# Optimization experiments

Hardware: AMD Instinct MI355X
Metric: run time of the kernel (lower is better)

The kernel has to match this reference:

```python
import jax, jax.numpy as jnp
import numpy as np

DIM = 3072
H = 24
HD = DIM // H  # 128
B = 1
IMG = 2048
TXT = 256


def _apply_rope(x, cos, sin):
    # x: [B, H, S, D]; cos/sin: [S, D]. Diffusers-style interleaved rotate-half:
    # pairs (x0, x1) -> (x0*c - x1*s, x1*c + x0*s)
    x1 = x[..., 0::2]
    x2 = x[..., 1::2]
    x_rot = jnp.stack([-x2, x1], axis=-1).reshape(x.shape)
    return x * cos + x_rot * sin


def setup_inputs() -> dict:
    key = jax.random.key(0)
    ks = jax.random.split(key, 26)

    def w(k):
        return jax.random.normal(k, (DIM, DIM), jnp.float32) * 0.02

    def b(k):
        return jax.random.normal(k, (DIM,), jnp.float32) * 0.02

    return {
        "image_hidden_states": jax.random.normal(ks[0], (B, IMG, DIM), jnp.float32),
        "text_hidden_states": jax.random.normal(ks[1], (B, TXT, DIM), jnp.float32),
        "img_cos": jax.random.uniform(ks[2], (IMG, HD), jnp.float32),
        "img_sin": jax.random.uniform(ks[3], (IMG, HD), jnp.float32),
        "txt_cos": jax.random.uniform(ks[4], (TXT, HD), jnp.float32),
        "txt_sin": jax.random.uniform(ks[5], (TXT, HD), jnp.float32),
        "Wq": w(ks[6]), "bq": b(ks[7]),
        "Wk": w(ks[8]), "bk": b(ks[9]),
        "Wv": w(ks[10]), "bv": b(ks[11]),
        "Waq": w(ks[12]), "baq": b(ks[13]),
        "Wak": w(ks[14]), "bak": b(ks[15]),
        "Wav": w(ks[16]), "bav": b(ks[17]),
        "Wo": w(ks[18]), "bo": b(ks[19]),
        "Wao": w(ks[20]), "bao": b(ks[21]),
    }


def reference(image_hidden_states, text_hidden_states, img_cos, img_sin,
              txt_cos, txt_sin, Wq, bq, Wk, bk, Wv, bv, Waq, baq, Wak, bak,
              Wav, bav, Wo, bo, Wao, bao):
    Bz, Si, D = image_hidden_states.shape
    St = text_hidden_states.shape[1]

    def proj(x, W, b):  # torch nn.Linear: x @ W.T + b
        return x @ W.T + b

    def heads(x, S):  # [B,S,D] -> [B,H,S,HD]
        return x.reshape(Bz, S, H, HD).transpose(0, 2, 1, 3)

    q_img = heads(proj(image_hidden_states, Wq, bq), Si)
    k_img = heads(proj(image_hidden_states, Wk, bk), Si)
    v_img = heads(proj(image_hidden_states, Wv, bv), Si)
    q_txt = heads(proj(text_hidden_states, Waq, baq), St)
    k_txt = heads(proj(text_hidden_states, Wak, bak), St)
    v_txt = heads(proj(text_hidden_states, Wav, bav), St)

    q_img = _apply_rope(q_img, img_cos, img_sin)
    k_img = _apply_rope(k_img, img_cos, img_sin)
    q_txt = _apply_rope(q_txt, txt_cos, txt_sin)
    k_txt = _apply_rope(k_txt, txt_cos, txt_sin)

    # joint sequence: text first, then image
    q = jnp.concatenate([q_txt, q_img], axis=2)
    k = jnp.concatenate([k_txt, k_img], axis=2)
    v = jnp.concatenate([v_txt, v_img], axis=2)

    scale = HD ** -0.5
    scores = jnp.einsum('bhqd,bhkd->bhqk', q, k) * scale  # [B,H,S,S]
    attn = jax.nn.softmax(scores, axis=-1)
    out = jnp.einsum('bhqk,bhkd->bhqd', attn, v)
    out = out.transpose(0, 2, 1, 3).reshape(Bz, St + Si, D)

    txt_out = out[:, :St] @ Wao.T + bao
    img_out = out[:, St:] @ Wo.T + bo
    return (img_out, txt_out)
```

## Files before the change

kernel.cpp:

```cpp
#include <hip/hip_runtime.h>
#include <cstdint>
#include <cstddef>

typedef __bf16 bf16x8 __attribute__((ext_vector_type(8)));
typedef float  f32x4  __attribute__((ext_vector_type(4)));

#define S_TXT 256
#define S_IMG 2048
#define S_TOT 2304
#define NHEAD 24
#define HDIM  128
#define DMODEL 3072

static constexpr size_t SZ_QKV  = (size_t)NHEAD * S_TOT * HDIM;
static constexpr size_t SZ_AO   = (size_t)S_TOT * DMODEL;
static constexpr size_t SZ_XIMG = (size_t)S_IMG * DMODEL;
static constexpr size_t SZ_XTXT = (size_t)S_TXT * DMODEL;
static constexpr size_t SZ_W    = (size_t)DMODEL * DMODEL;

__device__ __forceinline__ f32x4 mfma16(bf16x8 a, bf16x8 b, f32x4 c) {
  return __builtin_amdgcn_mfma_f32_16x16x32_bf16(a, b, c, 0, 0, 0);
}

__global__ __launch_bounds__(256) void cvt_f32_bf16(const float* __restrict__ in,
                                                    __bf16* __restrict__ out, int n) {
  int i = (blockIdx.x * 256 + threadIdx.x) * 8;
  if (i + 8 > n) return;
  f32x4 a = *(const f32x4*)(in + i);
  f32x4 b = *(const f32x4*)(in + i + 4);
  bf16x8 r;
  r[0]=(__bf16)a[0]; r[1]=(__bf16)a[1]; r[2]=(__bf16)a[2]; r[3]=(__bf16)a[3];
  r[4]=(__bf16)b[0]; r[5]=(__bf16)b[1]; r[6]=(__bf16)b[2]; r[7]=(__bf16)b[3];
  *(bf16x8*)(out + i) = r;
}

struct CWArgs { const float* s[6]; __bf16* d[6]; };
__global__ __launch_bounds__(256) void cvt_w(CWArgs a) {
  const float* in = a.s[blockIdx.y];
  __bf16* out = a.d[blockIdx.y];
  size_t i = ((size_t)blockIdx.x * 256 + threadIdx.x) * 8;
  f32x4 x = *(const f32x4*)(in + i);
  f32x4 y = *(const f32x4*)(in + i + 4);
  bf16x8 r;
  r[0]=(__bf16)x[0]; r[1]=(__bf16)x[1]; r[2]=(__bf16)x[2]; r[3]=(__bf16)x[3];
  r[4]=(__bf16)y[0]; r[5]=(__bf16)y[1]; r[6]=(__bf16)y[2]; r[7]=(__bf16)y[3];
  *(bf16x8*)(out + i) = r;
}

__global__ __launch_bounds__(256) void rope_kernel(__bf16* __restrict__ Qb, __bf16* __restrict__ Kb,
    const float* __restrict__ icos, const float* __restrict__ isin,
    const float* __restrict__ tcos, const float* __restrict__ tsin) {
  size_t idx = ((size_t)blockIdx.x * 256 + threadIdx.x) * 8;
  __bf16* X; float mult;
  if (blockIdx.y) { X = Kb; mult = 1.0f; }
  else            { X = Qb; mult = 0.08838834764831845f; }
  int d = (int)(idx & 127);
  int s = (int)((idx >> 7) % S_TOT);
  const float *cp, *sp; int ss;
  if (s < S_TXT) { cp = tcos; sp = tsin; ss = s; }
  else           { cp = icos; sp = isin; ss = s - S_TXT; }
  const float* cb = cp + (size_t)ss * HDIM + d;
  const float* sb = sp + (size_t)ss * HDIM + d;
  f32x4 c0 = *(const f32x4*)(cb);
  f32x4 c1 = *(const f32x4*)(cb + 4);
  f32x4 s0 = *(const f32x4*)(sb);
  f32x4 s1 = *(const f32x4*)(sb + 4);
  bf16x8 x = *(const bf16x8*)(X + idx);
  float xf[8];
  #pragma unroll
  for (int j = 0; j < 8; ++j) xf[j] = (float)x[j];
  bf16x8 o;
  o[0] = (__bf16)((xf[0]*c0[0] - xf[1]*s0[0]) * mult);
  o[1] = (__bf16)((xf[1]*c0[1] + xf[0]*s0[1]) * mult);
  o[2] = (__bf16)((xf[2]*c0[2] - xf[3]*s0[2]) * mult);
  o[3] = (__bf16)((xf[3]*c0[3] + xf[2]*s0[3]) * mult);
  o[4] = (__bf16)((xf[4]*c1[0] - xf[5]*s1[0]) * mult);
  o[5] = (__bf16)((xf[5]*c1[1] + xf[4]*s1[1]) * mult);
  o[6] = (__bf16)((xf[6]*c1[2] - xf[7]*s1[2]) * mult);
  o[7] = (__bf16)((xf[7]*c1[3] + xf[6]*s1[3]) * mult);
  *(bf16x8*)(X + idx) = o;
}

__global__ __launch_bounds__(128) void transpose_v(const __bf16* __restrict__ V,
                                                   __bf16* __restrict__ Vt) {
  int h = blockIdx.y, s0 = blockIdx.x * 64, d = threadIdx.x;
  const __bf16* src = V + ((size_t)h * S_TOT + s0) * HDIM + d;
  __bf16 tmp[64];
  #pragma unroll
  for (int k = 0; k < 64; ++k) tmp[k] = src[(size_t)k * HDIM];
  __bf16* dst = Vt + ((size_t)h * HDIM + d) * S_TOT + s0;
  #pragma unroll
  for (int k = 0; k < 8; ++k) {
    bf16x8 v;
    #pragma unroll
    for (int j = 0; j < 8; ++j) v[j] = tmp[k*8 + j];
    *(bf16x8*)(dst + k*8) = v;
  }
}

struct GBArgs {
  const __bf16* A;
  const __bf16* W0[3];
  const __bf16* W1[3];
  const float* b0[3]; const float* b1[3];
  void* O0[3]; void* O1[3];
};

template<int MODE>
__global__ __launch_bounds__(256) void gemm_bf(GBArgs ga) {
  const int tid = threadIdx.x;
  const int lane = tid & 63, wave = tid >> 6;
  const int wr = wave >> 1, wc = wave & 1;
  const int g = lane >> 4, lr = lane & 15;
  const int x7 = lr & 7;

  const int hw = (int)blockIdx.x;
  const int xcd = hw & 7, idx = hw >> 3;
  const int bx = idx % 18;
  const int nglob = (MODE == 0) ? (xcd * 9 + idx / 18) : (xcd * 3 + idx / 18);
  const int wsel = (MODE == 0) ? nglob / 24 : 0;
  const int ny   = (MODE == 0) ? nglob % 24 : nglob;
  const int m0 = bx * 128;
  const int n0 = ny * 128;
  const bool txt = (MODE == 0) ? (m0 >= S_IMG) : (m0 < S_TXT);
  const __bf16* Wf  = txt ? ga.W1[wsel] : ga.W0[wsel];
  const float* bias = txt ? ga.b1[wsel] : ga.b0[wsel];

  __shared__ __align__(16) __bf16 As[128 * 64];
  __shared__ __align__(16) __bf16 Bs[128 * 64];

  const int sr8 = lane >> 3;
  const int sch = (lane & 7) ^ sr8;
  const __bf16* Ap = ga.A + (size_t)(m0 + wave * 8 + sr8) * DMODEL + sch * 8;
  const __bf16* Bp = Wf   + (size_t)(n0 + wave * 8 + sr8) * DMODEL + sch * 8;

  f32x4 acc[4][4];
  #pragma unroll
  for (int i = 0; i < 4; ++i)
    #pragma unroll
    for (int j = 0; j < 4; ++j) acc[i][j] = (f32x4){0.f,0.f,0.f,0.f};

#define GLD(dst, srcp) { \
    _Pragma("unroll") \
    for (int i_ = 0; i_ < 4; ++i_) \
      __builtin_amdgcn_global_load_lds( \
          (const __attribute__((address_space(1))) void*)((srcp) + (size_t)i_ * 32 * DMODEL), \
          (__attribute__((address_space(3))) void*)((char*)(dst) + i_ * 4096 + wave * 1024), \
          16, 0, 0); }

  for (int kt = 0; kt < DMODEL / 64; ++kt) {
    GLD(As, Ap + kt * 64);
    GLD(Bs, Bp + kt * 64);
    __syncthreads();
    #pragma unroll
    for (int ks = 0; ks < 2; ++ks) {
      bf16x8 af[4], bf[4];
      #pragma unroll
      for (int i = 0; i < 4; ++i)
        af[i] = *(const bf16x8*)((char*)As + (wr*64 + i*16 + lr) * 128 + (((ks*4 + g) ^ x7) << 4));
      #pragma unroll
      for (int j = 0; j < 4; ++j)
        bf[j] = *(const bf16x8*)((char*)Bs + (wc*64 + j*16 + lr) * 128 + (((ks*4 + g) ^ x7) << 4));
      __builtin_amdgcn_s_setprio(1);
      #pragma unroll
      for (int i = 0; i < 4; ++i)
        #pragma unroll
        for (int j = 0; j < 4; ++j)
          acc[i][j] = mfma16(af[i], bf[j], acc[i][j]);
      __builtin_amdgcn_s_setprio(0);
    }
    __syncthreads();
  }
#undef GLD

  float bv[4];
  #pragma unroll
  for (int j = 0; j < 4; ++j) bv[j] = bias[n0 + wc*64 + j*16 + lr];

  if (MODE == 0) {
    __bf16* Qp = (__bf16*)(txt ? ga.O1[wsel] : ga.O0[wsel]);
    const int sbase = txt ? (m0 - S_IMG) : (m0 + S_TXT);
    #pragma unroll
    for (int i = 0; i < 4; ++i)
      #pragma unroll
      for (int j = 0; j < 4; ++j)
        #pragma unroll
        for (int r = 0; r < 4; ++r) {
          int s  = sbase + wr*64 + i*16 + g*4 + r;
          int hd = wc*64 + j*16 + lr;
          Qp[((size_t)ny * S_TOT + s) * HDIM + hd] = (__bf16)(acc[i][j][r] + bv[j]);
        }
  } else {
    float* Cf = (float*)(txt ? ga.O1[0] : ga.O0[0]);
    const int rbase = txt ? m0 : (m0 - S_TXT);
    #pragma unroll
    for (int i = 0; i < 4; ++i)
      #pragma unroll
      for (int j = 0; j < 4; ++j)
        #pragma unroll
        for (int r = 0; r < 4; ++r) {
          int m = rbase + wr*64 + i*16 + g*4 + r;
          int n = n0 + wc*64 + j*16 + lr;
          Cf[(size_t)m * DMODEL + n] = acc[i][j][r] + bv[j];
        }
  }
}

struct GArgs {
  const __bf16* A;
  const float* W0[3]; const float* W1[3];
  const float* b0[3]; const float* b1[3];
  void* O0[3]; void* O1[3];
};

#define NT 48

template<int MODE>
__global__ __launch_bounds__(256, 1) void gemm_all(GArgs ga) {
  const int tid = threadIdx.x;
  const int lane = tid & 63, wave = tid >> 6;
  const int wr = wave >> 1, wc = wave & 1;
  const int g = lane >> 4, lr = lane & 15;
  const int x7 = lr & 7;

  const int hw = (int)blockIdx.x;
  const int xcd = hw & 7, idx = hw >> 3;
  const int bx = idx % 18;
  const int nglob = (MODE == 0) ? (xcd * 9 + idx / 18) : (xcd * 3 + idx / 18);
  const int wsel = (MODE == 0) ? nglob / 24 : 0;
  const int ny   = (MODE == 0) ? nglob % 24 : nglob;
  const int m0 = bx * 128;
  const int n0 = ny * 128;
  const bool txt = (MODE == 0) ? (m0 >= S_IMG) : (m0 < S_TXT);
  const float* Wf   = txt ? ga.W1[wsel] : ga.W0[wsel];
  const float* bias = txt ? ga.b1[wsel] : ga.b0[wsel];

  __shared__ __align__(16) __bf16 As[2][128 * 64];
  __shared__ __align__(16) __bf16 Bs[128 * 64];

  const int sr8 = lane >> 3;
  const int sch = (lane & 7) ^ sr8;
  const __bf16* Ap = ga.A + (size_t)(m0 + wave * 8 + sr8) * DMODEL + sch * 8;

  const int wrow = tid >> 3;
  const int wch  = tid & 7;
  const float* Bp = Wf + (size_t)(n0 + wrow) * DMODEL + wch * 8;
  const int bwoff = wrow * 128 + ((wch ^ (wrow & 7)) << 4);

  f32x4 acc[4][4];
  #pragma unroll
  for (int i = 0; i < 4; ++i)
    #pragma unroll
    for (int j = 0; j < 4; ++j) acc[i][j] = (f32x4){0.f,0.f,0.f,0.f};

  f32x4 pre[4][2];

#define VSEP asm volatile("" ::: "memory")
#define ISSUE_A(kt, buf) { \
    const __bf16* Apk = Ap + (kt) * 64; \
    char* dst = (char*)(&As[(buf)][0]) + wave * 1024; \
    _Pragma("unroll") \
    for (int i_ = 0; i_ < 4; ++i_) \
      __builtin_amdgcn_global_load_lds( \
          (const __attribute__((address_space(1))) void*)(Apk + (size_t)i_ * 32 * DMODEL), \
          (__attribute__((address_space(3))) void*)(dst + i_ * 4096), 16, 0, 0); }
#define ISSUE_B(kt) { \
    const float* Bpk = Bp + (kt) * 64; \
    _Pragma("unroll") \
    for (int p_ = 0; p_ < 4; ++p_) { \
      pre[p_][0] = *(const f32x4*)(Bpk + (size_t)p_ * 32 * DMODEL); \
      pre[p_][1] = *(const f32x4*)(Bpk + (size_t)p_ * 32 * DMODEL + 4); } }
#define WRITE_B() { \
    _Pragma("unroll") \
    for (int p_ = 0; p_ < 4; ++p_) { \
      bf16x8 bw_; \
      _Pragma("unroll") \
      for (int j_ = 0; j_ < 4; ++j_) { \
        bw_[j_]     = (__bf16)pre[p_][0][j_]; \
        bw_[4 + j_] = (__bf16)pre[p_][1][j_]; } \
      *(bf16x8*)((char*)Bs + p_ * 4096 + bwoff) = bw_; } }
#define COMPUTE(buf) { \
    _Pragma("unroll") \
    for (int ks_ = 0; ks_ < 2; ++ks_) { \
      bf16x8 af_[4], bf_[4]; \
      _Pragma("unroll") \
      for (int i_ = 0; i_ < 4; ++i_) \
        af_[i_] = *(const bf16x8*)((char*)(&As[(buf)][0]) + (wr*64 + i_*16 + lr) * 128 + (((ks_*4 + g) ^ x7) << 4)); \
      _Pragma("unroll") \
      for (int j_ = 0; j_ < 4; ++j_) \
        bf_[j_] = *(const bf16x8*)((char*)Bs + (wc*64 + j_*16 + lr) * 128 + (((ks_*4 + g) ^ x7) << 4)); \
      __builtin_amdgcn_s_setprio(1); \
      _Pragma("unroll") \
      for (int i_ = 0; i_ < 4; ++i_) \
        _Pragma("unroll") \
        for (int j_ = 0; j_ < 4; ++j_) \
          acc[i_][j_] = mfma16(af_[i_], bf_[j_], acc[i_][j_]); \
      __builtin_amdgcn_s_setprio(0); } }

  ISSUE_B(0);        VSEP;
  ISSUE_A(0, 0);     VSEP;
  asm volatile("s_waitcnt vmcnt(4)" ::: "memory");
  WRITE_B();
  asm volatile("s_waitcnt vmcnt(0) lgkmcnt(0)" ::: "memory");
  __builtin_amdgcn_s_barrier();
  VSEP;

  for (int t = 0; t < NT - 2; t += 2) {
    ISSUE_A(t + 1, 1);  VSEP;
    ISSUE_B(t + 1);     VSEP;
    COMPUTE(0);
    __builtin_amdgcn_s_barrier();
    asm volatile("s_waitcnt vmcnt(0)" ::: "memory");
    WRITE_B();
    asm volatile("s_waitcnt lgkmcnt(0)" ::: "memory");
    __builtin_amdgcn_s_barrier();
    VSEP;
    ISSUE_A(t + 2, 0);  VSEP;
    ISSUE_B(t + 2);     VSEP;
    COMPUTE(1);
    __builtin_amdgcn_s_barrier();
    asm volatile("s_waitcnt vmcnt(0)" ::: "memory");
    WRITE_B();
    asm volatile("s_waitcnt lgkmcnt(0)" ::: "memory");
    __builtin_amdgcn_s_barrier();
    VSEP;
  }

  ISSUE_A(NT - 1, 1);  VSEP;
  ISSUE_B(NT - 1);     VSEP;
  COMPUTE(0);
  __builtin_amdgcn_s_barrier();
  asm volatile("s_waitcnt vmcnt(0)" ::: "memory");
  WRITE_B();
  asm volatile("s_waitcnt lgkmcnt(0)" ::: "memory");
  __builtin_amdgcn_s_barrier();
  COMPUTE(1);

#undef VSEP
#undef ISSUE_A
#undef ISSUE_B
#undef WRITE_B
#undef COMPUTE

  float bv[4];
  #pragma unroll
  for (int j = 0; j < 4; ++j) bv[j] = bias[n0 + wc*64 + j*16 + lr];

  if (MODE == 0) {
    __bf16* Qp = (__bf16*)(txt ? ga.O1[wsel] : ga.O0[wsel]);
    const int sbase = txt ? (m0 - S_IMG) : (m0 + S_TXT);
    #pragma unroll
    for (int i = 0; i < 4; ++i)
      #pragma unroll
      for (int j = 0; j < 4; ++j)
        #pragma unroll
        for (int r = 0; r < 4; ++r) {
          int s  = sbase + wr*64 + i*16 + g*4 + r;
          int hd = wc*64 + j*16 + lr;
          Qp[((size_t)ny * S_TOT + s) * HDIM + hd] = (__bf16)(acc[i][j][r] + bv[j]);
        }
  } else {
    float* Cf = (float*)(txt ? ga.O1[0] : ga.O0[0]);
    const int rbase = txt ? m0 : (m0 - S_TXT);
    #pragma unroll
    for (int i = 0; i < 4; ++i)
      #pragma unroll
      for (int j = 0; j < 4; ++j)
        #pragma unroll
        for (int r = 0; r < 4; ++r) {
          int m = rbase + wr*64 + i*16 + g*4 + r;
          int n = n0 + wc*64 + j*16 + lr;
          Cf[(size_t)m * DMODEL + n] = acc[i][j][r] + bv[j];
        }
  }
}

__global__ __launch_bounds__(256, 2) void flash_attn(
    const __bf16* __restrict__ Qg, const __bf16* __restrict__ Kg,
    const __bf16* __restrict__ Vt, __bf16* __restrict__ Og)
{
  const int h = blockIdx.y;
  const int q0 = blockIdx.x * 64;
  const int tid = threadIdx.x;
  const int lane = tid & 63, wave = tid >> 6;
  const int g = lane >> 4, lr = lane & 15;
  const int x7 = lr & 7;

  __shared__ __align__(16) __bf16 Kl[64 * 128];
  __shared__ __align__(16) __bf16 Vl[128 * 64];
  __shared__ __align__(16) __bf16 Pl[4][16 * 64];
  char* Kc = (char*)Kl;
  char* Vc = (char*)Vl;
  char* Pc = (char*)&Pl[wave][0];

  bf16x8 qf[4];
  {
    const __bf16* qp = Qg + ((size_t)h * S_TOT + q0 + wave*16 + lr) * HDIM + g * 8;
    #pragma unroll
    for (int kb = 0; kb < 4; ++kb) qf[kb] = *(const bf16x8*)(qp + kb * 32);
  }

  f32x4 acc[8];
  #pragma unroll
  for (int i = 0; i < 8; ++i) acc[i] = (f32x4){0.f,0.f,0.f,0.f};
  float mrow[4] = {-__builtin_inff(), -__builtin_inff(), -__builtin_inff(), -__builtin_inff()};
  float lrow[4] = {0.f, 0.f, 0.f, 0.f};

  const int krow = tid >> 4, kc = tid & 15;
  const int vrow = tid >> 3, vc = tid & 7;
  const __bf16* Kbase = Kg + (size_t)h * S_TOT * HDIM;
  const __bf16* Vbase = Vt + (size_t)h * HDIM * S_TOT;

  const int kwoff = krow * 256 + ((kc ^ (krow & 7)) << 4);
  const int vwoff = vrow * 128 + ((vc ^ (vrow & 7)) << 4);

  bf16x8 kreg[4], vreg[4];
  #pragma unroll
  for (int i = 0; i < 4; ++i) {
    kreg[i] = *(const bf16x8*)(Kbase + (size_t)(i*16 + krow) * HDIM + kc * 8);
    vreg[i] = *(const bf16x8*)(Vbase + (size_t)(i*32 + vrow) * S_TOT + vc * 8);
  }

  for (int t = 0; t < S_TOT / 64; ++t) {
    asm volatile("" ::: "memory");
    __builtin_amdgcn_s_barrier();
    asm volatile("" ::: "memory");
    #pragma unroll
    for (int i = 0; i < 4; ++i) {
      *(bf16x8*)(Kc + kwoff + i * 4096) = kreg[i];
      *(bf16x8*)(Vc + vwoff + i * 4096) = vreg[i];
    }
    if (t + 1 < S_TOT / 64) {
      int kv1 = (t + 1) * 64;
      #pragma unroll
      for (int i = 0; i < 4; ++i) {
        kreg[i] = *(const bf16x8*)(Kbase + (size_t)(kv1 + i*16 + krow) * HDIM + kc * 8);
        vreg[i] = *(const bf16x8*)(Vbase + (size_t)(i*32 + vrow) * S_TOT + kv1 + vc * 8);
      }
    }
    asm volatile("s_waitcnt lgkmcnt(0)" ::: "memory");
    __builtin_amdgcn_s_barrier();
    asm volatile("" ::: "memory");

    f32x4 sc[4];
    __builtin_amdgcn_s_setprio(1);
    #pragma unroll
    for (int kb = 0; kb < 4; ++kb) {
      f32x4 s4 = (f32x4){0.f,0.f,0.f,0.f};
      #pragma unroll
      for (int dk = 0; dk < 4; ++dk) {
        bf16x8 kf = *(const bf16x8*)(Kc + (kb*16 + lr) * 256 + (((dk*4 + g) ^ x7) << 4));
        s4 = mfma16(qf[dk], kf, s4);
      }
      sc[kb] = s4;
    }
    __builtin_amdgcn_s_setprio(0);

    float alpha[4];
    #pragma unroll
    for (int r = 0; r < 4; ++r) {
      float mx = fmaxf(fmaxf(sc[0][r], sc[1][r]), fmaxf(sc[2][r], sc[3][r]));
      mx = fmaxf(mx, __shfl_xor(mx, 1));
      mx = fmaxf(mx, __shfl_xor(mx, 2));
      mx = fmaxf(mx, __shfl_xor(mx, 4));
      mx = fmaxf(mx, __shfl_xor(mx, 8));
      float mn = fmaxf(mrow[r], mx);
      float al = __expf(mrow[r] - mn);
      mrow[r] = mn;
      float ps = 0.f;
      #pragma unroll
      for (int kb = 0; kb < 4; ++kb) {
        float p = __expf(sc[kb][r] - mn);
        sc[kb][r] = p;
        ps += p;
      }
      ps += __shfl_xor(ps, 1); ps += __shfl_xor(ps, 2);
      ps += __shfl_xor(ps, 4); ps += __shfl_xor(ps, 8);
      lrow[r] = lrow[r] * al + ps;
      alpha[r] = al;
    }

    #pragma unroll
    for (int kb = 0; kb < 4; ++kb)
      #pragma unroll
      for (int r = 0; r < 4; ++r) {
        int row = g*4 + r;
        *(__bf16*)(Pc + (((row * 128) + (kb*16 + lr) * 2) ^ ((row & 7) << 4))) = (__bf16)sc[kb][r];
      }

    #pragma unroll
    for (int db = 0; db < 8; ++db)
      #pragma unroll
      for (int r = 0; r < 4; ++r) acc[db][r] *= alpha[r];

    bf16x8 ap0 = *(const bf16x8*)(Pc + ((lr * 128 + g * 16) ^ (x7 << 4)));
    bf16x8 ap1 = *(const bf16x8*)(Pc + ((lr * 128 + (4 + g) * 16) ^ (x7 << 4)));
    __builtin_amdgcn_s_setprio(1);
    #pragma unroll
    for (int db = 0; db < 8; ++db) {
      bf16x8 v0 = *(const bf16x8*)(Vc + (db*16 + lr) * 128 + ((g ^ x7) << 4));
      bf16x8 v1 = *(const bf16x8*)(Vc + (db*16 + lr) * 128 + (((4 + g) ^ x7) << 4));
      acc[db] = mfma16(ap0, v0, acc[db]);
      acc[db] = mfma16(ap1, v1, acc[db]);
    }
    __builtin_amdgcn_s_setprio(0);
  }

  float rinv[4];
  #pragma unroll
  for (int r = 0; r < 4; ++r) rinv[r] = 1.f / lrow[r];
  #pragma unroll
  for (int db = 0; db < 8; ++db)
    #pragma unroll
    for (int r = 0; r < 4; ++r) {
      int s = q0 + wave*16 + g*4 + r;
      Og[(size_t)s * DMODEL + h * HDIM + db*16 + lr] = (__bf16)(acc[db][r] * rinv[r]);
    }
}

extern "C" void kernel_launch(void* const* d_in, const int* in_sizes, int n_in,
                              void* d_out, int out_size, void* d_ws, size_t ws_size,
                              hipStream_t stream) {
  const float* x_img   = (const float*)d_in[0];
  const float* x_txt   = (const float*)d_in[1];
  const float* img_cos = (const float*)d_in[2];
  const float* img_sin = (const float*)d_in[3];
  const float* txt_cos = (const float*)d_in[4];
  const float* txt_sin = (const float*)d_in[5];
  const float* Wq  = (const float*)d_in[6];  const float* bq  = (const float*)d_in[7];
  const float* Wk  = (const float*)d_in[8];  const float* bk  = (const float*)d_in[9];
  const float* Wv  = (const float*)d_in[10]; const float* bv  = (const float*)d_in[11];
  const float* Waq = (const float*)d_in[12]; const float* baq = (const float*)d_in[13];
  const float* Wak = (const float*)d_in[14]; const float* bak = (const float*)d_in[15];
  const float* Wav = (const float*)d_in[16]; const float* bav = (const float*)d_in[17];
  const float* Wo  = (const float*)d_in[18]; const float* bo  = (const float*)d_in[19];
  const float* Wao = (const float*)d_in[20]; const float* bao = (const float*)d_in[21];

  __bf16* ws = (__bf16*)d_ws;
  __bf16* Qb  = ws;
  __bf16* Kb  = Qb + SZ_QKV;
  __bf16* Vb  = Kb + SZ_QKV;
  __bf16* Vtb = Vb + SZ_QKV;
  __bf16* AO  = Vtb + SZ_QKV;
  __bf16* XI  = AO + SZ_AO;
  __bf16* XT  = XI + SZ_XIMG;
  __bf16* Wbf = XI + SZ_AO;

  const size_t need_big = (5 * SZ_QKV + SZ_AO + 6 * SZ_W) * sizeof(__bf16);
  const bool big = ws_size >= need_big;

  float* out_img = (float*)d_out;
  float* out_txt = out_img + (size_t)S_IMG * DMODEL;

  cvt_f32_bf16<<<dim3((unsigned)(SZ_XIMG/2048)), 256, 0, stream>>>(x_img, XI, (int)SZ_XIMG);
  cvt_f32_bf16<<<dim3((unsigned)(SZ_XTXT/2048)), 256, 0, stream>>>(x_txt, XT, (int)SZ_XTXT);

  if (big) {
    CWArgs cw{};
    const float* wsrc[6] = {Wq, Wk, Wv, Waq, Wak, Wav};
    for (int i = 0; i < 6; ++i) { cw.s[i] = wsrc[i]; cw.d[i] = Wbf + (size_t)i * SZ_W; }
    cvt_w<<<dim3((unsigned)(SZ_W/2048), 6), 256, 0, stream>>>(cw);

    GBArgs gb{};
    gb.A = XI;
    gb.W0[0] = Wbf;            gb.W0[1] = Wbf + SZ_W;     gb.W0[2] = Wbf + 2*SZ_W;
    gb.W1[0] = Wbf + 3*SZ_W;   gb.W1[1] = Wbf + 4*SZ_W;   gb.W1[2] = Wbf + 5*SZ_W;
    gb.b0[0] = bq;  gb.b0[1] = bk;  gb.b0[2] = bv;
    gb.b1[0] = baq; gb.b1[1] = bak; gb.b1[2] = bav;
    gb.O0[0] = Qb;  gb.O0[1] = Kb;  gb.O0[2] = Vb;
    gb.O1[0] = Qb;  gb.O1[1] = Kb;  gb.O1[2] = Vb;
    gemm_bf<0><<<dim3(1296), 256, 0, stream>>>(gb);
  } else {
    GArgs gq{};
    gq.A = XI;
    gq.W0[0] = Wq;  gq.W0[1] = Wk;  gq.W0[2] = Wv;
    gq.W1[0] = Waq; gq.W1[1] = Wak; gq.W1[2] = Wav;
    gq.b0[0] = bq;  gq.b0[1] = bk;  gq.b0[2] = bv;
    gq.b1[0] = baq; gq.b1[1] = bak; gq.b1[2] = bav;
    gq.O0[0] = Qb;  gq.O0[1] = Kb;  gq.O0[2] = Vb;
    gq.O1[0] = Qb;  gq.O1[1] = Kb;  gq.O1[2] = Vb;
    gemm_all<0><<<dim3(1296), 256, 0, stream>>>(gq);
  }

  rope_kernel<<<dim3(3456, 2), 256, 0, stream>>>(Qb, Kb, img_cos, img_sin, txt_cos, txt_sin);
  transpose_v<<<dim3(36, 24), 128, 0, stream>>>(Vb, Vtb);
  flash_attn<<<dim3(36, 24), 256, 0, stream>>>(Qb, Kb, Vtb, AO);

  if (big) {
    CWArgs cw{};
    cw.s[0] = Wo;  cw.d[0] = Wbf;
    cw.s[1] = Wao; cw.d[1] = Wbf + SZ_W;
    cvt_w<<<dim3((unsigned)(SZ_W/2048), 2), 256, 0, stream>>>(cw);

    GBArgs go{};
    go.A = AO;
    go.W0[0] = Wbf;       go.W1[0] = Wbf + SZ_W;
    go.b0[0] = bo;  go.b1[0] = bao;
    go.O0[0] = out_img; go.O1[0] = out_txt;
    gemm_bf<1><<<dim3(432), 256, 0, stream>>>(go);
  } else {
    GArgs go{};
    go.A = AO;
    go.W0[0] = Wo;  go.W1[0] = Wao;
    go.b0[0] = bo;  go.b1[0] = bao;
    go.O0[0] = out_img; go.O1[0] = out_txt;
    gemm_all<1><<<dim3(432), 256, 0, stream>>>(go);
  }

  (void)in_sizes; (void)n_in; (void)out_size;
}
```

Before: 473.8 us.

## Fuse RoPE and V transpose into QKV GEMM epilogue, use exp2 softmax

The QKV projection epilogue now applies RoPE, with the Q scale folded in, to Q and K directly. It also writes V already transposed, so in the bf16 path the separate rope and transpose kernels and their extra global round trips go away. The log2(e) factor is folded into the Q scale so the attention softmax can use exp2f instead of __expf. The trade-off is an epilogue that does scattered fp32 cos/sin loads, shuffles and strided bf16x4 V stores, which may cost more than the launches saved.

```diff
diff --git a/kernel.cpp b/kernel.cpp
--- a/kernel.cpp
+++ b/kernel.cpp
@@ -3,6 +3,7 @@
 #include <cstddef>
 
 typedef __bf16 bf16x8 __attribute__((ext_vector_type(8)));
+typedef __bf16 bf16x4 __attribute__((ext_vector_type(4)));
 typedef float  f32x4  __attribute__((ext_vector_type(4)));
 
 #define S_TXT 256
@@ -17,6 +18,8 @@
 static constexpr size_t SZ_XIMG = (size_t)S_IMG * DMODEL;
 static constexpr size_t SZ_XTXT = (size_t)S_TXT * DMODEL;
 static constexpr size_t SZ_W    = (size_t)DMODEL * DMODEL;
+
+#define QSCALE (0.08838834764831845f * 1.4426950408889634f)
 
 __device__ __forceinline__ f32x4 mfma16(bf16x8 a, bf16x8 b, f32x4 c) {
   return __builtin_amdgcn_mfma_f32_16x16x32_bf16(a, b, c, 0, 0, 0);
@@ -53,7 +56,7 @@
   size_t idx = ((size_t)blockIdx.x * 256 + threadIdx.x) * 8;
   __bf16* X; float mult;
   if (blockIdx.y) { X = Kb; mult = 1.0f; }
-  else            { X = Qb; mult = 0.08838834764831845f; }
+  else            { X = Qb; mult = QSCALE; }
   int d = (int)(idx & 127);
   int s = (int)((idx >> 7) % S_TOT);
   const float *cp, *sp; int ss;
@@ -104,6 +107,8 @@
   const __bf16* W1[3];
   const float* b0[3]; const float* b1[3];
   void* O0[3]; void* O1[3];
+  const float* icos; const float* isin;
+  const float* tcos; const float* tsin;
 };
 
 template<int MODE>
@@ -178,18 +183,47 @@
   for (int j = 0; j < 4; ++j) bv[j] = bias[n0 + wc*64 + j*16 + lr];
 
   if (MODE == 0) {
-    __bf16* Qp = (__bf16*)(txt ? ga.O1[wsel] : ga.O0[wsel]);
-    const int sbase = txt ? (m0 - S_IMG) : (m0 + S_TXT);
-    #pragma unroll
-    for (int i = 0; i < 4; ++i)
-      #pragma unroll
-      for (int j = 0; j < 4; ++j)
+    const int head = ny;
+    if (wsel == 2) {
+      __bf16* Vt = (__bf16*)ga.O0[2];
+      const int sbase = txt ? (m0 - S_IMG) : (m0 + S_TXT);
+      #pragma unroll
+      for (int i = 0; i < 4; ++i) {
+        const int s0 = sbase + wr*64 + i*16 + g*4;
         #pragma unroll
-        for (int r = 0; r < 4; ++r) {
-          int s  = sbase + wr*64 + i*16 + g*4 + r;
-          int hd = wc*64 + j*16 + lr;
-          Qp[((size_t)ny * S_TOT + s) * HDIM + hd] = (__bf16)(acc[i][j][r] + bv[j]);
+        for (int j = 0; j < 4; ++j) {
+          const int hd = wc*64 + j*16 + lr;
+          bf16x4 pk;
+          #pragma unroll
+          for (int r = 0; r < 4; ++r) pk[r] = (__bf16)(acc[i][j][r] + bv[j]);
+          *(bf16x4*)(Vt + ((size_t)(head * HDIM + hd)) * S_TOT + s0) = pk;
         }
+      }
+    } else {
+      __bf16* Qp = (__bf16*)ga.O0[wsel];
+      const float* tc = txt ? ga.tcos : ga.icos;
+      const float* ts = txt ? ga.tsin : ga.isin;
+      const float mult = (wsel == 0) ? QSCALE : 1.0f;
+      const int sbase = txt ? (m0 - S_IMG) : (m0 + S_TXT);
+      const int tbase = txt ? (m0 - S_IMG) : m0;
+      #pragma unroll
+      for (int i = 0; i < 4; ++i)
+        #pragma unroll
+        for (int j = 0; j < 4; ++j) {
+          const int hd = wc*64 + j*16 + lr;
+          #pragma unroll
+          for (int r = 0; r < 4; ++r) {
+            const int soff = wr*64 + i*16 + g*4 + r;
+            float v = acc[i][j][r] + bv[j];
+            float p = __shfl_xor(v, 1);
+            const size_t trow = (size_t)(tbase + soff) * HDIM + hd;
+            float c  = tc[trow];
+            float sn = ts[trow];
+            float o = (lr & 1) ? (v * c + p * sn) : (v * c - p * sn);
+            Qp[((size_t)head * S_TOT + (sbase + soff)) * HDIM + hd] = (__bf16)(o * mult);
+          }
+        }
+    }
   } else {
     float* Cf = (float*)(txt ? ga.O1[0] : ga.O0[0]);
     const int rbase = txt ? m0 : (m0 - S_TXT);
@@ -465,12 +499,12 @@
       mx = fmaxf(mx, __shfl_xor(mx, 4));
       mx = fmaxf(mx, __shfl_xor(mx, 8));
       float mn = fmaxf(mrow[r], mx);
-      float al = __expf(mrow[r] - mn);
+      float al = exp2f(mrow[r] - mn);
       mrow[r] = mn;
       float ps = 0.f;
       #pragma unroll
       for (int kb = 0; kb < 4; ++kb) {
-        float p = __expf(sc[kb][r] - mn);
+        float p = exp2f(sc[kb][r] - mn);
         sc[kb][r] = p;
         ps += p;
       }
@@ -567,8 +601,9 @@
     gb.W1[0] = Wbf + 3*SZ_W;   gb.W1[1] = Wbf + 4*SZ_W;   gb.W1[2] = Wbf + 5*SZ_W;
     gb.b0[0] = bq;  gb.b0[1] = bk;  gb.b0[2] = bv;
     gb.b1[0] = baq; gb.b1[1] = bak; gb.b1[2] = bav;
-    gb.O0[0] = Qb;  gb.O0[1] = Kb;  gb.O0[2] = Vb;
-    gb.O1[0] = Qb;  gb.O1[1] = Kb;  gb.O1[2] = Vb;
+    gb.O0[0] = Qb;  gb.O0[1] = Kb;  gb.O0[2] = Vtb;
+    gb.O1[0] = Qb;  gb.O1[1] = Kb;  gb.O1[2] = Vtb;
+    gb.icos = img_cos; gb.isin = img_sin; gb.tcos = txt_cos; gb.tsin = txt_sin;
     gemm_bf<0><<<dim3(1296), 256, 0, stream>>>(gb);
   } else {
     GArgs gq{};
@@ -580,10 +615,10 @@
     gq.O0[0] = Qb;  gq.O0[1] = Kb;  gq.O0[2] = Vb;
     gq.O1[0] = Qb;  gq.O1[1] = Kb;  gq.O1[2] = Vb;
     gemm_all<0><<<dim3(1296), 256, 0, stream>>>(gq);
-  }
-
-  rope_kernel<<<dim3(3456, 2), 256, 0, stream>>>(Qb, Kb, img_cos, img_sin, txt_cos, txt_sin);
-  transpose_v<<<dim3(36, 24), 128, 0, stream>>>(Vb, Vtb);
+    rope_kernel<<<dim3(3456, 2), 256, 0, stream>>>(Qb, Kb, img_cos, img_sin, txt_cos, txt_sin);
+    transpose_v<<<dim3(36, 24), 128, 0, stream>>>(Vb, Vtb);
+  }
+
   flash_attn<<<dim3(36, 24), 256, 0, stream>>>(Qb, Kb, Vtb, AO);
 
   if (big) {
```

Result: slower. 506.4 us (+6.9%).
